# Performance work log

Hardware: AMD Instinct MI355X
Metric: run time of the kernel (lower is better)

The kernel has to match this reference:

```python
import jax, jax.numpy as jnp
import numpy as np

B, N, E = 4, 50000, 800000
C_IN, C_OUT, K = 64, 64, 3  # K = max_degree
AVG_DEG = 16.0


def setup_inputs() -> dict:
    key = jax.random.key(0)
    k1, k2, k3, k4, k5 = jax.random.split(key, 5)
    x = jax.random.normal(k1, (B, N, C_IN), dtype=jnp.float32)
    lap_rows = jax.random.randint(k2, (E,), 0, N)
    lap_cols = jax.random.randint(k3, (E,), 0, N)
    # scale so ||L|| stays O(1) and the Chebyshev recursion is stable
    lap_vals = jax.random.normal(k4, (E,), dtype=jnp.float32) / AVG_DEG
    weights = jax.random.normal(k5, (K + 1, C_IN, C_OUT), dtype=jnp.float32) * 0.1
    bias = jnp.full((C_OUT,), 0.1, dtype=jnp.float32)
    return dict(x=x, lap_rows=lap_rows, lap_cols=lap_cols,
                lap_vals=lap_vals, weights=weights, bias=bias)


def reference(x, lap_rows, lap_cols, lap_vals, weights, bias):
    # Sparse L @ X via edge list: gather source rows, scale, scatter-add to dest rows.
    def spmm_one(xb):  # xb: [N, C]
        return jax.ops.segment_sum(lap_vals[:, None] * xb[lap_cols], lap_rows,
                                   num_segments=N)

    spmm = jax.vmap(spmm_one)  # [B, N, C] -> [B, N, C]

    Tx0 = x
    out = jnp.einsum('bnc,co->bno', Tx0, weights[0])
    Tx1 = spmm(Tx0)
    out = out + jnp.einsum('bnc,co->bno', Tx1, weights[1])
    for k in range(2, K + 1):
        Tx2 = 2.0 * spmm(Tx1) - Tx0
        out = out + jnp.einsum('bnc,co->bno', Tx2, weights[k])
        Tx0, Tx1 = Tx1, Tx2
    return jax.nn.relu(out + bias)
```

## Files before the change

### kernel.cpp

```cpp
#include <hip/hip_runtime.h>


#define N_NODES 50000
#define N_EDGES 800000
#define BATCH 4
#define CH 64
#define BN (N_NODES * CH)
#define ROWS_TOTAL (BATCH * N_NODES)
#define NB 782
#define EPB 8192
#define SCT_BLOCKS ((N_EDGES + EPB - 1) / EPB)

typedef unsigned int uint;
typedef unsigned short ushort;
typedef unsigned char uchar;
typedef __attribute__((ext_vector_type(8))) short short8;
typedef __attribute__((ext_vector_type(4))) float f32x4;

__device__ __forceinline__ uint pack_bf16(float lo, float hi) {
  uint a = __float_as_uint(lo);
  uint b = __float_as_uint(hi);
  a = (a + 0x7fffu + ((a >> 16) & 1u)) >> 16;
  b = (b + 0x7fffu + ((b >> 16) & 1u)) >> 16;
  return a | (b << 16);
}
__device__ __forceinline__ ushort bf16one(float x) {
  uint a = __float_as_uint(x);
  a = (a + 0x7fffu + ((a >> 16) & 1u)) >> 16;
  return (ushort)a;
}
__device__ __forceinline__ uint q_u8(float v, float inv) {
  return (uint)((int)rintf(v * inv) + 128) & 0xffu;
}

__global__ __launch_bounds__(1024) void bucket_hist(const int* __restrict__ rows,
                                                    int* __restrict__ gcounts) {
  __shared__ int h[NB];
  for (int b = threadIdx.x; b < NB; b += 1024) h[b] = 0;
  __syncthreads();
  int base_e = blockIdx.x * EPB;
#pragma unroll
  for (int j = 0; j < EPB / 1024; ++j) {
    int e = base_e + j * 1024 + threadIdx.x;
    if (e < N_EDGES) atomicAdd(&h[rows[e] >> 6], 1);
  }
  __syncthreads();
  for (int b = threadIdx.x; b < NB; b += 1024)
    if (h[b]) atomicAdd(&gcounts[b], h[b]);
}

__global__ __launch_bounds__(1024) void bucket_scan(const int* __restrict__ gcounts,
                                                    int* __restrict__ bucket_base,
                                                    int* __restrict__ gcursor) {
  __shared__ int s[1024];
  int t = threadIdx.x;
  int v = (t < NB) ? gcounts[t] : 0;
  s[t] = v;
  __syncthreads();
  for (int off = 1; off < 1024; off <<= 1) {
    int tv = (t >= off) ? s[t - off] : 0;
    __syncthreads();
    s[t] += tv;
    __syncthreads();
  }
  int ex = s[t] - v;
  if (t < NB) { bucket_base[t] = ex; gcursor[t] = ex; }
  if (t == NB) bucket_base[NB] = N_EDGES;
}

__global__ __launch_bounds__(1024) void bucket_scatter(const int* __restrict__ rows,
                                                       const int* __restrict__ cols,
                                                       const float* __restrict__ vals,
                                                       int* __restrict__ gcursor,
                                                       uint2* __restrict__ staging) {
  __shared__ int lcur[NB];
  for (int b = threadIdx.x; b < NB; b += 1024) lcur[b] = 0;
  __syncthreads();
  int base_e = blockIdx.x * EPB;
#pragma unroll
  for (int j = 0; j < EPB / 1024; ++j) {
    int e = base_e + j * 1024 + threadIdx.x;
    if (e < N_EDGES) atomicAdd(&lcur[rows[e] >> 6], 1);
  }
  __syncthreads();
  for (int b = threadIdx.x; b < NB; b += 1024) {
    int c = lcur[b];
    lcur[b] = (c > 0) ? atomicAdd(&gcursor[b], c) : 0;
  }
  __syncthreads();
#pragma unroll
  for (int j = 0; j < EPB / 1024; ++j) {
    int e = base_e + j * 1024 + threadIdx.x;
    if (e < N_EDGES) {
      int r = rows[e];
      int pos = atomicAdd(&lcur[r >> 6], 1);
      staging[pos] = make_uint2((uint)cols[e] | ((uint)(r & 63) << 20),
                                __float_as_uint(vals[e]));
    }
  }
}

__global__ __launch_bounds__(256) void bucket_finalize(const int* __restrict__ bucket_base,
                                                       const uint2* __restrict__ staging,
                                                       uint2* __restrict__ pairs,
                                                       int* __restrict__ row_start) {
  int b = blockIdx.x;
  int seg0 = bucket_base[b], seg1 = bucket_base[b + 1];
  __shared__ int hist[64];
  __shared__ int cur[64];
  if (threadIdx.x < 64) hist[threadIdx.x] = 0;
  __syncthreads();
  for (int i = seg0 + threadIdx.x; i < seg1; i += 256)
    atomicAdd(&hist[staging[i].x >> 20], 1);
  __syncthreads();
  if (threadIdx.x < 64) {
    int v = hist[threadIdx.x];
    int sc = v;
#pragma unroll
    for (int off = 1; off < 64; off <<= 1) {
      int t = __shfl_up(sc, off, 64);
      if (threadIdx.x >= (unsigned)off) sc += t;
    }
    int start = seg0 + sc - v;
    cur[threadIdx.x] = start;
    int r = b * 64 + threadIdx.x;
    if (r < N_NODES) row_start[r] = start;
    if (r == N_NODES) row_start[N_NODES] = N_EDGES;
  }
  __syncthreads();
  for (int i = seg0 + threadIdx.x; i < seg1; i += 256) {
    uint2 eu = staging[i];
    int rl = eu.x >> 20;
    int pos = atomicAdd(&cur[rl], 1);
    pairs[pos] = make_uint2(eu.x & 0xFFFFFu, eu.y);
  }
}

__global__ __launch_bounds__(256) void wprep_kernel(const float* __restrict__ w,
                                                    ushort* __restrict__ wtT) {
  int t = blockIdx.x * 256 + threadIdx.x;
  if (t >= 64 * 256) return;
  int o = t >> 8, k = t & 255, m = k >> 6, c = k & 63;
  int idx = c * 64 + o;
  float v;
  if (m == 0)      v = w[idx] - w[2 * 4096 + idx];
  else if (m == 1) v = w[4096 + idx] - 3.0f * w[3 * 4096 + idx];
  else if (m == 2) v = 2.0f * w[2 * 4096 + idx];
  else             v = 4.0f * w[3 * 4096 + idx];
  wtT[t] = bf16one(v);
}

__global__ __launch_bounds__(256) void cvt_kernel(const float* __restrict__ in,
                                                  uint* __restrict__ xb,
                                                  uint* __restrict__ xu8w,
                                                  float* __restrict__ xsc) {
  int node = blockIdx.x * 4 + (threadIdx.x >> 6);
  int lane = threadIdx.x & 63;
  int b = lane >> 4;
  int ch4 = (lane & 15) * 4;
  float4 v = *reinterpret_cast<const float4*>(in + (size_t)b * BN + (size_t)node * 64 + ch4);
  uint2 bw = make_uint2(pack_bf16(v.x, v.y), pack_bf16(v.z, v.w));
  *reinterpret_cast<uint2*>(xb + (size_t)node * 128 + b * 32 + (lane & 15) * 2) = bw;
  float mx = fmaxf(fmaxf(fabsf(v.x), fabsf(v.y)), fmaxf(fabsf(v.z), fabsf(v.w)));
#pragma unroll
  for (int off = 1; off < 64; off <<= 1) mx = fmaxf(mx, __shfl_xor(mx, off, 64));
  float inv = mx > 0.f ? 127.0f / mx : 0.f;
  uint w8 = q_u8(v.x, inv) | (q_u8(v.y, inv) << 8) |
            (q_u8(v.z, inv) << 16) | (q_u8(v.w, inv) << 24);
  xu8w[(size_t)node * 64 + lane] = w8;
  if (lane == 0) xsc[node] = mx * (1.0f / 127.0f);
}

__device__ __forceinline__ void fma16_u8(float acc[16], float& sm, float m,
                                         const uint4& w) {
  const uint arr[4] = {w.x, w.y, w.z, w.w};
#pragma unroll
  for (int t = 0; t < 4; ++t) {
    uint u = arr[t];
    acc[t * 4 + 0] = fmaf(m, (float)(u & 0xffu),         acc[t * 4 + 0]);
    acc[t * 4 + 1] = fmaf(m, (float)((u >> 8) & 0xffu),  acc[t * 4 + 1]);
    acc[t * 4 + 2] = fmaf(m, (float)((u >> 16) & 0xffu), acc[t * 4 + 2]);
    acc[t * 4 + 3] = fmaf(m, (float)(u >> 24),           acc[t * 4 + 3]);
  }
  sm += m;
}

__device__ __forceinline__ void spmm_body(const int* __restrict__ row_start,
                                          const uint2* __restrict__ pairs,
                                          const uchar* __restrict__ src,
                                          const float* __restrict__ ssc,
                                          uchar* __restrict__ dst,
                                          float* __restrict__ dsc) {
  int row = blockIdx.x * 4 + (threadIdx.x >> 6);
  int lane = threadIdx.x & 63;
  int q = lane >> 4;
  int ql = lane & 15;
  const uchar* sb = src + ql * 16;
  int s = row_start[row], e = row_start[row + 1];
  float acc[16];
  float sm = 0.f;
#pragma unroll
  for (int j = 0; j < 16; ++j) acc[j] = 0.f;
  int i = s;
  for (; i + 7 < e; i += 8) {
    uint2 pa = pairs[i + q];
    uint2 pb = pairs[i + 4 + q];
    uint4 qa = *reinterpret_cast<const uint4*>(sb + (size_t)pa.x * 256);
    uint4 qb = *reinterpret_cast<const uint4*>(sb + (size_t)pb.x * 256);
    float ma = __uint_as_float(pa.y) * ssc[pa.x];
    float mb = __uint_as_float(pb.y) * ssc[pb.x];
    fma16_u8(acc, sm, ma, qa);
    fma16_u8(acc, sm, mb, qb);
  }
  for (; i < e; i += 4) {
    if (i + q < e) {
      uint2 p0 = pairs[i + q];
      uint4 q0 = *reinterpret_cast<const uint4*>(sb + (size_t)p0.x * 256);
      fma16_u8(acc, sm, __uint_as_float(p0.y) * ssc[p0.x], q0);
    }
  }
#pragma unroll
  for (int j = 0; j < 16; ++j) {
    acc[j] += __shfl_xor(acc[j], 16, 64);
    acc[j] += __shfl_xor(acc[j], 32, 64);
  }
  sm += __shfl_xor(sm, 16, 64);
  sm += __shfl_xor(sm, 32, 64);
#pragma unroll
  for (int j = 0; j < 16; ++j) acc[j] = fmaf(-128.f, sm, acc[j]);
  float mx = 0.f;
#pragma unroll
  for (int j = 0; j < 16; ++j) mx = fmaxf(mx, fabsf(acc[j]));
#pragma unroll
  for (int off = 1; off < 16; off <<= 1) mx = fmaxf(mx, __shfl_xor(mx, off, 64));
  if (lane < 16) {
    float inv = mx > 0.f ? 127.0f / mx : 0.f;
    uint w[4];
#pragma unroll
    for (int t = 0; t < 4; ++t) {
      w[t] = q_u8(acc[t * 4 + 0], inv) | (q_u8(acc[t * 4 + 1], inv) << 8) |
             (q_u8(acc[t * 4 + 2], inv) << 16) | (q_u8(acc[t * 4 + 3], inv) << 24);
    }
    *reinterpret_cast<uint4*>(dst + (size_t)row * 256 + ql * 16) =
        make_uint4(w[0], w[1], w[2], w[3]);
    if (lane == 0) dsc[row] = mx * (1.0f / 127.0f);
  }
}

__global__ __launch_bounds__(256) void spmm_s1(const int* __restrict__ rs,
                                               const uint2* __restrict__ pr,
                                               const uchar* __restrict__ src,
                                               const float* __restrict__ ssc,
                                               uchar* __restrict__ dst,
                                               float* __restrict__ dsc) {
  spmm_body(rs, pr, src, ssc, dst, dsc);
}
__global__ __launch_bounds__(256) void spmm_s2(const int* __restrict__ rs,
                                               const uint2* __restrict__ pr,
                                               const uchar* __restrict__ src,
                                               const float* __restrict__ ssc,
                                               uchar* __restrict__ dst,
                                               float* __restrict__ dsc) {
  spmm_body(rs, pr, src, ssc, dst, dsc);
}
__global__ __launch_bounds__(256) void spmm_s3(const int* __restrict__ rs,
                                               const uint2* __restrict__ pr,
                                               const uchar* __restrict__ src,
                                               const float* __restrict__ ssc,
                                               uchar* __restrict__ dst,
                                               float* __restrict__ dsc) {
  spmm_body(rs, pr, src, ssc, dst, dsc);
}

__device__ __forceinline__ short8 dequant8_u8(uint2 q, float sc, float nb) {
  float f0 = fmaf((float)(q.x & 0xffu),         sc, nb);
  float f1 = fmaf((float)((q.x >> 8) & 0xffu),  sc, nb);
  float f2 = fmaf((float)((q.x >> 16) & 0xffu), sc, nb);
  float f3 = fmaf((float)(q.x >> 24),           sc, nb);
  float f4 = fmaf((float)(q.y & 0xffu),         sc, nb);
  float f5 = fmaf((float)((q.y >> 8) & 0xffu),  sc, nb);
  float f6 = fmaf((float)((q.y >> 16) & 0xffu), sc, nb);
  float f7 = fmaf((float)(q.y >> 24),           sc, nb);
  uint4 v = make_uint4(pack_bf16(f0, f1), pack_bf16(f2, f3),
                       pack_bf16(f4, f5), pack_bf16(f6, f7));
  return __builtin_bit_cast(short8, v);
}

__global__ __launch_bounds__(256) void gemm4_mfma(
    const uint* __restrict__ A0bf,
    const uchar* __restrict__ A1u8, const float* __restrict__ A1sc,
    const uchar* __restrict__ A2u8, const float* __restrict__ A2sc,
    const uchar* __restrict__ A3u8, const float* __restrict__ A3sc,
    const uint* __restrict__ wtT,
    const float* __restrict__ bias, float* __restrict__ out) {
  __shared__ uint WS[64 * 132];
  __shared__ float bias_s[64];
  for (int w = threadIdx.x; w < 8192; w += 256)
    WS[(w >> 7) * 132 + (w & 127)] = wtT[w];
  if (threadIdx.x < 64) bias_s[threadIdx.x] = bias[threadIdx.x];
  __syncthreads();

  const int lane = threadIdx.x & 63;
  const int wv = threadIdx.x >> 6;
  const int r0 = blockIdx.x * 64 + wv * 16;
  const int c16 = lane & 15;
  const int hi = lane >> 4;

  const int ar = r0 + c16;
  const size_t arow_w = (size_t)ar * 32 + hi * 4;
  const size_t arow_b = (size_t)ar * 64 + hi * 8;
  const int nd = ar >> 2;
  const float sc1 = A1sc[nd];
  const float sc2 = A2sc[nd];
  const float sc3 = A3sc[nd];

  f32x4 acc[4] = {{0.f, 0.f, 0.f, 0.f}, {0.f, 0.f, 0.f, 0.f},
                  {0.f, 0.f, 0.f, 0.f}, {0.f, 0.f, 0.f, 0.f}};

#pragma unroll
  for (int ks = 0; ks < 8; ++ks) {
    short8 afrag;
    const int m = ks >> 1;
    if (m == 0) {
      uint4 av = *reinterpret_cast<const uint4*>(A0bf + arow_w + (ks & 1) * 16);
      afrag = __builtin_bit_cast(short8, av);
    } else if (m == 1) {
      uint2 qv = *reinterpret_cast<const uint2*>(A1u8 + arow_b + (ks & 1) * 32);
      afrag = dequant8_u8(qv, sc1, -128.f * sc1);
    } else if (m == 2) {
      uint2 qv = *reinterpret_cast<const uint2*>(A2u8 + arow_b + (ks & 1) * 32);
      afrag = dequant8_u8(qv, sc2, -128.f * sc2);
    } else {
      uint2 qv = *reinterpret_cast<const uint2*>(A3u8 + arow_b + (ks & 1) * 32);
      afrag = dequant8_u8(qv, sc3, -128.f * sc3);
    }
#pragma unroll
    for (int nt = 0; nt < 4; ++nt) {
      uint4 bv = *reinterpret_cast<const uint4*>(
          &WS[(nt * 16 + c16) * 132 + ks * 16 + hi * 4]);
      short8 bfrag = __builtin_bit_cast(short8, bv);
      acc[nt] = __builtin_amdgcn_mfma_f32_16x16x32_bf16(afrag, bfrag, acc[nt], 0, 0, 0);
    }
  }

#pragma unroll
  for (int nt = 0; nt < 4; ++nt) {
#pragma unroll
    for (int i = 0; i < 4; ++i) {
      int row = r0 + hi * 4 + i;
      int node = row >> 2, b = row & 3;
      int col = nt * 16 + c16;
      float v = acc[nt][i] + bias_s[col];
      out[(size_t)b * BN + (size_t)node * 64 + col] = fmaxf(v, 0.f);
    }
  }
}

extern "C" void kernel_launch(void* const* d_in, const int* in_sizes, int n_in,
                              void* d_out, int out_size, void* d_ws, size_t ws_size,
                              hipStream_t stream) {
  const float* x        = (const float*)d_in[0];
  const int*   lap_rows = (const int*)d_in[1];
  const int*   lap_cols = (const int*)d_in[2];
  const float* lap_vals = (const float*)d_in[3];
  const float* weights  = (const float*)d_in[4];
  const float* bias     = (const float*)d_in[5];
  float* out = (float*)d_out;

  char* ws = (char*)d_ws;
  size_t off = 0;
  auto alloc = [&](size_t bytes) {
    void* p = ws + off;
    off += (bytes + 255) & ~(size_t)255;
    return p;
  };
  int*    gcounts     = (int*)alloc((size_t)NB * 4);
  int*    gcursor     = (int*)alloc((size_t)NB * 4);
  int*    bucket_base = (int*)alloc((size_t)(NB + 1) * 4);
  int*    row_start   = (int*)alloc((size_t)(N_NODES + 1) * 4);
  uint2*  pairs       = (uint2*)alloc((size_t)N_EDGES * 8);
  uint2*  staging     = (uint2*)alloc((size_t)N_EDGES * 8);
  ushort* wtT         = (ushort*)alloc((size_t)64 * 256 * 2);
  uint*   xb          = (uint*)alloc((size_t)N_NODES * 128 * 4);
  uchar*  xu8         = (uchar*)alloc((size_t)N_NODES * 256);
  uchar*  S1u         = (uchar*)alloc((size_t)N_NODES * 256);
  uchar*  S2u         = (uchar*)alloc((size_t)N_NODES * 256);
  uchar*  S3u         = (uchar*)alloc((size_t)N_NODES * 256);
  float*  xsc         = (float*)alloc((size_t)N_NODES * 4);
  float*  S1sc        = (float*)alloc((size_t)N_NODES * 4);
  float*  S2sc        = (float*)alloc((size_t)N_NODES * 4);
  float*  S3sc        = (float*)alloc((size_t)N_NODES * 4);
  (void)ws_size; (void)in_sizes; (void)n_in; (void)out_size;

  wprep_kernel<<<64, 256, 0, stream>>>(weights, wtT);
  cvt_kernel<<<N_NODES / 4, 256, 0, stream>>>(x, xb, (uint*)xu8, xsc);
  hipMemsetAsync(gcounts, 0, (size_t)NB * 4, stream);
  bucket_hist<<<SCT_BLOCKS, 1024, 0, stream>>>(lap_rows, gcounts);
  bucket_scan<<<1, 1024, 0, stream>>>(gcounts, bucket_base, gcursor);
  bucket_scatter<<<SCT_BLOCKS, 1024, 0, stream>>>(lap_rows, lap_cols, lap_vals,
                                                  gcursor, staging);
  bucket_finalize<<<NB, 256, 0, stream>>>(bucket_base, staging, pairs, row_start);

  const int spmm_blocks = N_NODES / 4;

  spmm_s1<<<spmm_blocks, 256, 0, stream>>>(row_start, pairs, xu8, xsc, S1u, S1sc);
  spmm_s2<<<spmm_blocks, 256, 0, stream>>>(row_start, pairs, S1u, S1sc, S2u, S2sc);
  spmm_s3<<<spmm_blocks, 256, 0, stream>>>(row_start, pairs, S2u, S2sc, S3u, S3sc);
  gemm4_mfma<<<ROWS_TOTAL / 64, 256, 0, stream>>>(xb, S1u, S1sc, S2u, S2sc,
                                                  S3u, S3sc, (const uint*)wtT,
                                                  bias, out);
}
```

Measured before the change: 194.2 us.

## Split quantized feature rows into four channel slabs with per-slab scales

Node features are now quantized to u8 in four 64-byte slabs (per batch, 16 channels each), each with its own scale, stored as separate planes. The SpMM grid grows fourfold so each block handles one slab, gathering 4 bytes per lane instead of 16. A smaller working set per plane is meant to give better cache locality for the random gathers. The cost is more per-edge index and scale loads, and the GEMM has to read scales from several planes. Finer-grained scales also change the quantization precision.

```diff
diff --git a/kernel.cpp b/kernel.cpp
--- a/kernel.cpp
+++ b/kernel.cpp
@@ -10,6 +10,10 @@
 #define NB 782
 #define EPB 8192
 #define SCT_BLOCKS ((N_EDGES + EPB - 1) / EPB)
+#define NSUB 4
+#define SUB_BLOCKS (N_NODES / 4)
+#define RW (N_NODES * 16)
+#define RB (N_NODES * 64)
 
 typedef unsigned int uint;
 typedef unsigned short ushort;
@@ -157,117 +161,112 @@
   int node = blockIdx.x * 4 + (threadIdx.x >> 6);
   int lane = threadIdx.x & 63;
   int b = lane >> 4;
-  int ch4 = (lane & 15) * 4;
-  float4 v = *reinterpret_cast<const float4*>(in + (size_t)b * BN + (size_t)node * 64 + ch4);
+  int c4 = (lane & 15) * 4;
+  float4 v = *reinterpret_cast<const float4*>(in + (size_t)b * BN + (size_t)node * 64 + c4);
   uint2 bw = make_uint2(pack_bf16(v.x, v.y), pack_bf16(v.z, v.w));
   *reinterpret_cast<uint2*>(xb + (size_t)node * 128 + b * 32 + (lane & 15) * 2) = bw;
   float mx = fmaxf(fmaxf(fabsf(v.x), fabsf(v.y)), fmaxf(fabsf(v.z), fabsf(v.w)));
-#pragma unroll
-  for (int off = 1; off < 64; off <<= 1) mx = fmaxf(mx, __shfl_xor(mx, off, 64));
+  mx = fmaxf(mx, __shfl_xor(mx, 1, 64));
+  mx = fmaxf(mx, __shfl_xor(mx, 2, 64));
+  mx = fmaxf(mx, __shfl_xor(mx, 16, 64));
+  mx = fmaxf(mx, __shfl_xor(mx, 32, 64));
   float inv = mx > 0.f ? 127.0f / mx : 0.f;
   uint w8 = q_u8(v.x, inv) | (q_u8(v.y, inv) << 8) |
             (q_u8(v.z, inv) << 16) | (q_u8(v.w, inv) << 24);
-  xu8w[(size_t)node * 64 + lane] = w8;
-  if (lane == 0) xsc[node] = mx * (1.0f / 127.0f);
-}
-
-__device__ __forceinline__ void fma16_u8(float acc[16], float& sm, float m,
-                                         const uint4& w) {
-  const uint arr[4] = {w.x, w.y, w.z, w.w};
-#pragma unroll
-  for (int t = 0; t < 4; ++t) {
-    uint u = arr[t];
-    acc[t * 4 + 0] = fmaf(m, (float)(u & 0xffu),         acc[t * 4 + 0]);
-    acc[t * 4 + 1] = fmaf(m, (float)((u >> 8) & 0xffu),  acc[t * 4 + 1]);
-    acc[t * 4 + 2] = fmaf(m, (float)((u >> 16) & 0xffu), acc[t * 4 + 2]);
-    acc[t * 4 + 3] = fmaf(m, (float)(u >> 24),           acc[t * 4 + 3]);
-  }
+  int k = (lane & 15) >> 2;
+  xu8w[(size_t)k * RW + (size_t)node * 16 + b * 4 + (lane & 3)] = w8;
+  if ((lane & 51) == 0)
+    xsc[k * N_NODES + node] = mx * (1.0f / 127.0f);
+}
+
+__device__ __forceinline__ void fma4_u8(float acc[4], float& sm, float m, uint u) {
+  acc[0] = fmaf(m, (float)(u & 0xffu),         acc[0]);
+  acc[1] = fmaf(m, (float)((u >> 8) & 0xffu),  acc[1]);
+  acc[2] = fmaf(m, (float)((u >> 16) & 0xffu), acc[2]);
+  acc[3] = fmaf(m, (float)(u >> 24),           acc[3]);
   sm += m;
 }
 
 __device__ __forceinline__ void spmm_body(const int* __restrict__ row_start,
                                           const uint2* __restrict__ pairs,
-                                          const uchar* __restrict__ src,
+                                          const uint* __restrict__ src,
                                           const float* __restrict__ ssc,
-                                          uchar* __restrict__ dst,
+                                          uint* __restrict__ dst,
                                           float* __restrict__ dsc) {
-  int row = blockIdx.x * 4 + (threadIdx.x >> 6);
+  int k = blockIdx.x / SUB_BLOCKS;
+  int nc = blockIdx.x - k * SUB_BLOCKS;
+  int row = nc * 4 + (threadIdx.x >> 6);
   int lane = threadIdx.x & 63;
   int q = lane >> 4;
   int ql = lane & 15;
-  const uchar* sb = src + ql * 16;
+  const uint* srcl = src + (size_t)k * RW + ql;
+  const float* sscl = ssc + k * N_NODES;
   int s = row_start[row], e = row_start[row + 1];
-  float acc[16];
+  float acc[4] = {0.f, 0.f, 0.f, 0.f};
   float sm = 0.f;
-#pragma unroll
-  for (int j = 0; j < 16; ++j) acc[j] = 0.f;
   int i = s;
   for (; i + 7 < e; i += 8) {
     uint2 pa = pairs[i + q];
     uint2 pb = pairs[i + 4 + q];
-    uint4 qa = *reinterpret_cast<const uint4*>(sb + (size_t)pa.x * 256);
-    uint4 qb = *reinterpret_cast<const uint4*>(sb + (size_t)pb.x * 256);
-    float ma = __uint_as_float(pa.y) * ssc[pa.x];
-    float mb = __uint_as_float(pb.y) * ssc[pb.x];
-    fma16_u8(acc, sm, ma, qa);
-    fma16_u8(acc, sm, mb, qb);
+    uint ua = srcl[(size_t)pa.x * 16];
+    uint ub = srcl[(size_t)pb.x * 16];
+    float ma = __uint_as_float(pa.y) * sscl[pa.x];
+    float mb = __uint_as_float(pb.y) * sscl[pb.x];
+    fma4_u8(acc, sm, ma, ua);
+    fma4_u8(acc, sm, mb, ub);
   }
   for (; i < e; i += 4) {
     if (i + q < e) {
       uint2 p0 = pairs[i + q];
-      uint4 q0 = *reinterpret_cast<const uint4*>(sb + (size_t)p0.x * 256);
-      fma16_u8(acc, sm, __uint_as_float(p0.y) * ssc[p0.x], q0);
-    }
-  }
-#pragma unroll
-  for (int j = 0; j < 16; ++j) {
+      uint u0 = srcl[(size_t)p0.x * 16];
+      fma4_u8(acc, sm, __uint_as_float(p0.y) * sscl[p0.x], u0);
+    }
+  }
+#pragma unroll
+  for (int j = 0; j < 4; ++j) {
     acc[j] += __shfl_xor(acc[j], 16, 64);
     acc[j] += __shfl_xor(acc[j], 32, 64);
   }
   sm += __shfl_xor(sm, 16, 64);
   sm += __shfl_xor(sm, 32, 64);
 #pragma unroll
-  for (int j = 0; j < 16; ++j) acc[j] = fmaf(-128.f, sm, acc[j]);
-  float mx = 0.f;
-#pragma unroll
-  for (int j = 0; j < 16; ++j) mx = fmaxf(mx, fabsf(acc[j]));
-#pragma unroll
-  for (int off = 1; off < 16; off <<= 1) mx = fmaxf(mx, __shfl_xor(mx, off, 64));
+  for (int j = 0; j < 4; ++j) acc[j] = fmaf(-128.f, sm, acc[j]);
+  float mx = fmaxf(fmaxf(fabsf(acc[0]), fabsf(acc[1])),
+                   fmaxf(fabsf(acc[2]), fabsf(acc[3])));
+  mx = fmaxf(mx, __shfl_xor(mx, 1, 64));
+  mx = fmaxf(mx, __shfl_xor(mx, 2, 64));
+  mx = fmaxf(mx, __shfl_xor(mx, 4, 64));
+  mx = fmaxf(mx, __shfl_xor(mx, 8, 64));
   if (lane < 16) {
     float inv = mx > 0.f ? 127.0f / mx : 0.f;
-    uint w[4];
-#pragma unroll
-    for (int t = 0; t < 4; ++t) {
-      w[t] = q_u8(acc[t * 4 + 0], inv) | (q_u8(acc[t * 4 + 1], inv) << 8) |
-             (q_u8(acc[t * 4 + 2], inv) << 16) | (q_u8(acc[t * 4 + 3], inv) << 24);
-    }
-    *reinterpret_cast<uint4*>(dst + (size_t)row * 256 + ql * 16) =
-        make_uint4(w[0], w[1], w[2], w[3]);
-    if (lane == 0) dsc[row] = mx * (1.0f / 127.0f);
+    uint w = q_u8(acc[0], inv) | (q_u8(acc[1], inv) << 8) |
+             (q_u8(acc[2], inv) << 16) | (q_u8(acc[3], inv) << 24);
+    dst[(size_t)k * RW + (size_t)row * 16 + ql] = w;
+    if (lane == 0) dsc[k * N_NODES + row] = mx * (1.0f / 127.0f);
   }
 }
 
 __global__ __launch_bounds__(256) void spmm_s1(const int* __restrict__ rs,
                                                const uint2* __restrict__ pr,
-                                               const uchar* __restrict__ src,
+                                               const uint* __restrict__ src,
                                                const float* __restrict__ ssc,
-                                               uchar* __restrict__ dst,
+                                               uint* __restrict__ dst,
                                                float* __restrict__ dsc) {
   spmm_body(rs, pr, src, ssc, dst, dsc);
 }
 __global__ __launch_bounds__(256) void spmm_s2(const int* __restrict__ rs,
                                                const uint2* __restrict__ pr,
-                                               const uchar* __restrict__ src,
+                                               const uint* __restrict__ src,
                                                const float* __restrict__ ssc,
-                                               uchar* __restrict__ dst,
+                                               uint* __restrict__ dst,
                                                float* __restrict__ dsc) {
   spmm_body(rs, pr, src, ssc, dst, dsc);
 }
 __global__ __launch_bounds__(256) void spmm_s3(const int* __restrict__ rs,
                                                const uint2* __restrict__ pr,
-                                               const uchar* __restrict__ src,
+                                               const uint* __restrict__ src,
                                                const float* __restrict__ ssc,
-                                               uchar* __restrict__ dst,
+                                               uint* __restrict__ dst,
                                                float* __restrict__ dsc) {
   spmm_body(rs, pr, src, ssc, dst, dsc);
 }
@@ -305,14 +304,20 @@
   const int r0 = blockIdx.x * 64 + wv * 16;
   const int c16 = lane & 15;
   const int hi = lane >> 4;
+  const int hv = hi >> 1;
+  const int hb = (hi & 1) * 8;
 
   const int ar = r0 + c16;
   const size_t arow_w = (size_t)ar * 32 + hi * 4;
-  const size_t arow_b = (size_t)ar * 64 + hi * 8;
-  const int nd = ar >> 2;
-  const float sc1 = A1sc[nd];
-  const float sc2 = A2sc[nd];
-  const float sc3 = A3sc[nd];
+  const int node = ar >> 2, bb = ar & 3;
+  const size_t abase = (size_t)node * 64 + bb * 16 + hb;
+
+  float s1r0 = A1sc[node], s1r1 = A1sc[N_NODES + node],
+        s1r2 = A1sc[2 * N_NODES + node], s1r3 = A1sc[3 * N_NODES + node];
+  float s2r0 = A2sc[node], s2r1 = A2sc[N_NODES + node],
+        s2r2 = A2sc[2 * N_NODES + node], s2r3 = A2sc[3 * N_NODES + node];
+  float s3r0 = A3sc[node], s3r1 = A3sc[N_NODES + node],
+        s3r2 = A3sc[2 * N_NODES + node], s3r3 = A3sc[3 * N_NODES + node];
 
   f32x4 acc[4] = {{0.f, 0.f, 0.f, 0.f}, {0.f, 0.f, 0.f, 0.f},
                   {0.f, 0.f, 0.f, 0.f}, {0.f, 0.f, 0.f, 0.f}};
@@ -321,18 +326,19 @@
   for (int ks = 0; ks < 8; ++ks) {
     short8 afrag;
     const int m = ks >> 1;
+    const int kk = ks & 1;
     if (m == 0) {
-      uint4 av = *reinterpret_cast<const uint4*>(A0bf + arow_w + (ks & 1) * 16);
+      uint4 av = *reinterpret_cast<const uint4*>(A0bf + arow_w + kk * 16);
       afrag = __builtin_bit_cast(short8, av);
-    } else if (m == 1) {
-      uint2 qv = *reinterpret_cast<const uint2*>(A1u8 + arow_b + (ks & 1) * 32);
-      afrag = dequant8_u8(qv, sc1, -128.f * sc1);
-    } else if (m == 2) {
-      uint2 qv = *reinterpret_cast<const uint2*>(A2u8 + arow_b + (ks & 1) * 32);
-      afrag = dequant8_u8(qv, sc2, -128.f * sc2);
     } else {
-      uint2 qv = *reinterpret_cast<const uint2*>(A3u8 + arow_b + (ks & 1) * 32);
-      afrag = dequant8_u8(qv, sc3, -128.f * sc3);
+      const uchar* Au = (m == 1) ? A1u8 : (m == 2) ? A2u8 : A3u8;
+      float sc;
+      if (m == 1) sc = kk ? (hv ? s1r3 : s1r2) : (hv ? s1r1 : s1r0);
+      else if (m == 2) sc = kk ? (hv ? s2r3 : s2r2) : (hv ? s2r1 : s2r0);
+      else sc = kk ? (hv ? s3r3 : s3r2) : (hv ? s3r1 : s3r0);
+      const int kreg = kk * 2 + hv;
+      uint2 qv = *reinterpret_cast<const uint2*>(Au + (size_t)kreg * RB + abase);
+      afrag = dequant8_u8(qv, sc, -128.f * sc);
     }
 #pragma unroll
     for (int nt = 0; nt < 4; ++nt) {
@@ -348,10 +354,10 @@
 #pragma unroll
     for (int i = 0; i < 4; ++i) {
       int row = r0 + hi * 4 + i;
-      int node = row >> 2, b = row & 3;
+      int nd2 = row >> 2, b2 = row & 3;
       int col = nt * 16 + c16;
       float v = acc[nt][i] + bias_s[col];
-      out[(size_t)b * BN + (size_t)node * 64 + col] = fmaxf(v, 0.f);
+      out[(size_t)b2 * BN + (size_t)nd2 * 64 + col] = fmaxf(v, 0.f);
     }
   }
 }
@@ -382,18 +388,18 @@
   uint2*  staging     = (uint2*)alloc((size_t)N_EDGES * 8);
   ushort* wtT         = (ushort*)alloc((size_t)64 * 256 * 2);
   uint*   xb          = (uint*)alloc((size_t)N_NODES * 128 * 4);
-  uchar*  xu8         = (uchar*)alloc((size_t)N_NODES * 256);
-  uchar*  S1u         = (uchar*)alloc((size_t)N_NODES * 256);
-  uchar*  S2u         = (uchar*)alloc((size_t)N_NODES * 256);
-  uchar*  S3u         = (uchar*)alloc((size_t)N_NODES * 256);
-  float*  xsc         = (float*)alloc((size_t)N_NODES * 4);
-  float*  S1sc        = (float*)alloc((size_t)N_NODES * 4);
-  float*  S2sc        = (float*)alloc((size_t)N_NODES * 4);
-  float*  S3sc        = (float*)alloc((size_t)N_NODES * 4);
+  uint*   xu8         = (uint*)alloc((size_t)NSUB * RW * 4);
+  uint*   S1u         = (uint*)alloc((size_t)NSUB * RW * 4);
+  uint*   S2u         = (uint*)alloc((size_t)NSUB * RW * 4);
+  uint*   S3u         = (uint*)alloc((size_t)NSUB * RW * 4);
+  float*  xsc         = (float*)alloc((size_t)NSUB * N_NODES * 4);
+  float*  S1sc        = (float*)alloc((size_t)NSUB * N_NODES * 4);
+  float*  S2sc        = (float*)alloc((size_t)NSUB * N_NODES * 4);
+  float*  S3sc        = (float*)alloc((size_t)NSUB * N_NODES * 4);
   (void)ws_size; (void)in_sizes; (void)n_in; (void)out_size;
 
   wprep_kernel<<<64, 256, 0, stream>>>(weights, wtT);
-  cvt_kernel<<<N_NODES / 4, 256, 0, stream>>>(x, xb, (uint*)xu8, xsc);
+  cvt_kernel<<<N_NODES / 4, 256, 0, stream>>>(x, xb, xu8, xsc);
   hipMemsetAsync(gcounts, 0, (size_t)NB * 4, stream);
   bucket_hist<<<SCT_BLOCKS, 1024, 0, stream>>>(lap_rows, gcounts);
   bucket_scan<<<1, 1024, 0, stream>>>(gcounts, bucket_base, gcursor);
@@ -401,12 +407,13 @@
                                                   gcursor, staging);
   bucket_finalize<<<NB, 256, 0, stream>>>(bucket_base, staging, pairs, row_start);
 
-  const int spmm_blocks = N_NODES / 4;
-
-  spmm_s1<<<spmm_blocks, 256, 0, stream>>>(row_start, pairs, xu8, xsc, S1u, S1sc);
-  spmm_s2<<<spmm_blocks, 256, 0, stream>>>(row_start, pairs, S1u, S1sc, S2u, S2sc);
-  spmm_s3<<<spmm_blocks, 256, 0, stream>>>(row_start, pairs, S2u, S2sc, S3u, S3sc);
-  gemm4_mfma<<<ROWS_TOTAL / 64, 256, 0, stream>>>(xb, S1u, S1sc, S2u, S2sc,
-                                                  S3u, S3sc, (const uint*)wtT,
-                                                  bias, out);
-}
+  const int spmm_grid = NSUB * SUB_BLOCKS;
+
+  spmm_s1<<<spmm_grid, 256, 0, stream>>>(row_start, pairs, xu8, xsc, S1u, S1sc);
+  spmm_s2<<<spmm_grid, 256, 0, stream>>>(row_start, pairs, S1u, S1sc, S2u, S2sc);
+  spmm_s3<<<spmm_grid, 256, 0, stream>>>(row_start, pairs, S2u, S2sc, S3u, S3sc);
+  gemm4_mfma<<<ROWS_TOTAL / 64, 256, 0, stream>>>(xb, (const uchar*)S1u, S1sc,
+                                                  (const uchar*)S2u, S2sc,
+                                                  (const uchar*)S3u, S3sc,
+                                                  (const uint*)wtT, bias, out);
+}
```

After: 336.3 us. 1.73x slower.

## Prescale edge values by source scales and drop bf16 copy of input

Applied to the files above, without the earlier changes.

Adds a scale_pairs kernel that multiplies each edge value by its source node's quantization scale before each SpMM. The SpMM inner loop then no longer performs a random gather of the scale array. The input is also stored only as u8, in a batch-major layout, and the GEMM dequantizes term 0 the same way as the other terms, so the bf16 x buffer is no longer written or read. The cost is three extra passes over the 6.4MB edge array, and term 0 now feeds the MMA from 8-bit values instead of bf16, which lowers its precision.

```diff
diff --git a/kernel.cpp b/kernel.cpp
--- a/kernel.cpp
+++ b/kernel.cpp
@@ -134,6 +134,15 @@
     int pos = atomicAdd(&cur[rl], 1);
     pairs[pos] = make_uint2(eu.x & 0xFFFFFu, eu.y);
   }
+}
+
+__global__ __launch_bounds__(256) void scale_pairs(const uint2* __restrict__ raw,
+                                                   const float* __restrict__ sc,
+                                                   uint2* __restrict__ outp) {
+  int e = blockIdx.x * 256 + threadIdx.x;
+  if (e >= N_EDGES) return;
+  uint2 p = raw[e];
+  outp[e] = make_uint2(p.x, __float_as_uint(__uint_as_float(p.y) * sc[p.x]));
 }
 
 __global__ __launch_bounds__(256) void wprep_kernel(const float* __restrict__ w,
@@ -151,23 +160,20 @@
 }
 
 __global__ __launch_bounds__(256) void cvt_kernel(const float* __restrict__ in,
-                                                  uint* __restrict__ xb,
                                                   uint* __restrict__ xu8w,
                                                   float* __restrict__ xsc) {
   int node = blockIdx.x * 4 + (threadIdx.x >> 6);
   int lane = threadIdx.x & 63;
   int b = lane >> 4;
-  int ch4 = (lane & 15) * 4;
-  float4 v = *reinterpret_cast<const float4*>(in + (size_t)b * BN + (size_t)node * 64 + ch4);
-  uint2 bw = make_uint2(pack_bf16(v.x, v.y), pack_bf16(v.z, v.w));
-  *reinterpret_cast<uint2*>(xb + (size_t)node * 128 + b * 32 + (lane & 15) * 2) = bw;
+  int c4 = (lane & 15) * 4;
+  float4 v = *reinterpret_cast<const float4*>(in + (size_t)b * BN + (size_t)node * 64 + c4);
   float mx = fmaxf(fmaxf(fabsf(v.x), fabsf(v.y)), fmaxf(fabsf(v.z), fabsf(v.w)));
 #pragma unroll
   for (int off = 1; off < 64; off <<= 1) mx = fmaxf(mx, __shfl_xor(mx, off, 64));
   float inv = mx > 0.f ? 127.0f / mx : 0.f;
   uint w8 = q_u8(v.x, inv) | (q_u8(v.y, inv) << 8) |
             (q_u8(v.z, inv) << 16) | (q_u8(v.w, inv) << 24);
-  xu8w[(size_t)node * 64 + lane] = w8;
+  xu8w[(size_t)node * 64 + b * 16 + (lane & 15)] = w8;
   if (lane == 0) xsc[node] = mx * (1.0f / 127.0f);
 }
 
@@ -188,7 +194,6 @@
 __device__ __forceinline__ void spmm_body(const int* __restrict__ row_start,
                                           const uint2* __restrict__ pairs,
                                           const uchar* __restrict__ src,
-                                          const float* __restrict__ ssc,
                                           uchar* __restrict__ dst,
                                           float* __restrict__ dsc) {
   int row = blockIdx.x * 4 + (threadIdx.x >> 6);
@@ -207,16 +212,14 @@
     uint2 pb = pairs[i + 4 + q];
     uint4 qa = *reinterpret_cast<const uint4*>(sb + (size_t)pa.x * 256);
     uint4 qb = *reinterpret_cast<const uint4*>(sb + (size_t)pb.x * 256);
-    float ma = __uint_as_float(pa.y) * ssc[pa.x];
-    float mb = __uint_as_float(pb.y) * ssc[pb.x];
-    fma16_u8(acc, sm, ma, qa);
-    fma16_u8(acc, sm, mb, qb);
+    fma16_u8(acc, sm, __uint_as_float(pa.y), qa);
+    fma16_u8(acc, sm, __uint_as_float(pb.y), qb);
   }
   for (; i < e; i += 4) {
     if (i + q < e) {
       uint2 p0 = pairs[i + q];
       uint4 q0 = *reinterpret_cast<const uint4*>(sb + (size_t)p0.x * 256);
-      fma16_u8(acc, sm, __uint_as_float(p0.y) * ssc[p0.x], q0);
+      fma16_u8(acc, sm, __uint_as_float(p0.y), q0);
     }
   }
 #pragma unroll
@@ -250,26 +253,23 @@
 __global__ __launch_bounds__(256) void spmm_s1(const int* __restrict__ rs,
                                                const uint2* __restrict__ pr,
                                                const uchar* __restrict__ src,
-                                               const float* __restrict__ ssc,
                                                uchar* __restrict__ dst,
                                                float* __restrict__ dsc) {
-  spmm_body(rs, pr, src, ssc, dst, dsc);
+  spmm_body(rs, pr, src, dst, dsc);
 }
 __global__ __launch_bounds__(256) void spmm_s2(const int* __restrict__ rs,
                                                const uint2* __restrict__ pr,
                                                const uchar* __restrict__ src,
-                                               const float* __restrict__ ssc,
                                                uchar* __restrict__ dst,
                                                float* __restrict__ dsc) {
-  spmm_body(rs, pr, src, ssc, dst, dsc);
+  spmm_body(rs, pr, src, dst, dsc);
 }
 __global__ __launch_bounds__(256) void spmm_s3(const int* __restrict__ rs,
                                                const uint2* __restrict__ pr,
                                                const uchar* __restrict__ src,
-                                               const float* __restrict__ ssc,
                                                uchar* __restrict__ dst,
                                                float* __restrict__ dsc) {
-  spmm_body(rs, pr, src, ssc, dst, dsc);
+  spmm_body(rs, pr, src, dst, dsc);
 }
 
 __device__ __forceinline__ short8 dequant8_u8(uint2 q, float sc, float nb) {
@@ -287,7 +287,7 @@
 }
 
 __global__ __launch_bounds__(256) void gemm4_mfma(
-    const uint* __restrict__ A0bf,
+    const uchar* __restrict__ A0u8, const float* __restrict__ A0sc,
     const uchar* __restrict__ A1u8, const float* __restrict__ A1sc,
     const uchar* __restrict__ A2u8, const float* __restrict__ A2sc,
     const uchar* __restrict__ A3u8, const float* __restrict__ A3sc,
@@ -307,9 +307,9 @@
   const int hi = lane >> 4;
 
   const int ar = r0 + c16;
-  const size_t arow_w = (size_t)ar * 32 + hi * 4;
   const size_t arow_b = (size_t)ar * 64 + hi * 8;
   const int nd = ar >> 2;
+  const float sc0 = A0sc[nd];
   const float sc1 = A1sc[nd];
   const float sc2 = A2sc[nd];
   const float sc3 = A3sc[nd];
@@ -319,21 +319,11 @@
 
 #pragma unroll
   for (int ks = 0; ks < 8; ++ks) {
-    short8 afrag;
     const int m = ks >> 1;
-    if (m == 0) {
-      uint4 av = *reinterpret_cast<const uint4*>(A0bf + arow_w + (ks & 1) * 16);
-      afrag = __builtin_bit_cast(short8, av);
-    } else if (m == 1) {
-      uint2 qv = *reinterpret_cast<const uint2*>(A1u8 + arow_b + (ks & 1) * 32);
-      afrag = dequant8_u8(qv, sc1, -128.f * sc1);
-    } else if (m == 2) {
-      uint2 qv = *reinterpret_cast<const uint2*>(A2u8 + arow_b + (ks & 1) * 32);
-      afrag = dequant8_u8(qv, sc2, -128.f * sc2);
-    } else {
-      uint2 qv = *reinterpret_cast<const uint2*>(A3u8 + arow_b + (ks & 1) * 32);
-      afrag = dequant8_u8(qv, sc3, -128.f * sc3);
-    }
+    const uchar* Au = (m == 0) ? A0u8 : (m == 1) ? A1u8 : (m == 2) ? A2u8 : A3u8;
+    const float sc = (m == 0) ? sc0 : (m == 1) ? sc1 : (m == 2) ? sc2 : sc3;
+    uint2 qv = *reinterpret_cast<const uint2*>(Au + arow_b + (ks & 1) * 32);
+    short8 afrag = dequant8_u8(qv, sc, -128.f * sc);
 #pragma unroll
     for (int nt = 0; nt < 4; ++nt) {
       uint4 bv = *reinterpret_cast<const uint4*>(
@@ -378,10 +368,11 @@
   int*    gcursor     = (int*)alloc((size_t)NB * 4);
   int*    bucket_base = (int*)alloc((size_t)(NB + 1) * 4);
   int*    row_start   = (int*)alloc((size_t)(N_NODES + 1) * 4);
-  uint2*  pairs       = (uint2*)alloc((size_t)N_EDGES * 8);
+  uint2*  pairs_raw   = (uint2*)alloc((size_t)N_EDGES * 8);
+  uint2*  pairs_a     = (uint2*)alloc((size_t)N_EDGES * 8);
+  uint2*  pairs_b     = (uint2*)alloc((size_t)N_EDGES * 8);
   uint2*  staging     = (uint2*)alloc((size_t)N_EDGES * 8);
   ushort* wtT         = (ushort*)alloc((size_t)64 * 256 * 2);
-  uint*   xb          = (uint*)alloc((size_t)N_NODES * 128 * 4);
   uchar*  xu8         = (uchar*)alloc((size_t)N_NODES * 256);
   uchar*  S1u         = (uchar*)alloc((size_t)N_NODES * 256);
   uchar*  S2u         = (uchar*)alloc((size_t)N_NODES * 256);
@@ -393,20 +384,24 @@
   (void)ws_size; (void)in_sizes; (void)n_in; (void)out_size;
 
   wprep_kernel<<<64, 256, 0, stream>>>(weights, wtT);
-  cvt_kernel<<<N_NODES / 4, 256, 0, stream>>>(x, xb, (uint*)xu8, xsc);
+  cvt_kernel<<<N_NODES / 4, 256, 0, stream>>>(x, (uint*)xu8, xsc);
   hipMemsetAsync(gcounts, 0, (size_t)NB * 4, stream);
   bucket_hist<<<SCT_BLOCKS, 1024, 0, stream>>>(lap_rows, gcounts);
   bucket_scan<<<1, 1024, 0, stream>>>(gcounts, bucket_base, gcursor);
   bucket_scatter<<<SCT_BLOCKS, 1024, 0, stream>>>(lap_rows, lap_cols, lap_vals,
                                                   gcursor, staging);
-  bucket_finalize<<<NB, 256, 0, stream>>>(bucket_base, staging, pairs, row_start);
+  bucket_finalize<<<NB, 256, 0, stream>>>(bucket_base, staging, pairs_raw, row_start);
 
   const int spmm_blocks = N_NODES / 4;
-
-  spmm_s1<<<spmm_blocks, 256, 0, stream>>>(row_start, pairs, xu8, xsc, S1u, S1sc);
-  spmm_s2<<<spmm_blocks, 256, 0, stream>>>(row_start, pairs, S1u, S1sc, S2u, S2sc);
-  spmm_s3<<<spmm_blocks, 256, 0, stream>>>(row_start, pairs, S2u, S2sc, S3u, S3sc);
-  gemm4_mfma<<<ROWS_TOTAL / 64, 256, 0, stream>>>(xb, S1u, S1sc, S2u, S2sc,
+  const int sp_blocks = (N_EDGES + 255) / 256;
+
+  scale_pairs<<<sp_blocks, 256, 0, stream>>>(pairs_raw, xsc, pairs_a);
+  spmm_s1<<<spmm_blocks, 256, 0, stream>>>(row_start, pairs_a, xu8, S1u, S1sc);
+  scale_pairs<<<sp_blocks, 256, 0, stream>>>(pairs_raw, S1sc, pairs_b);
+  spmm_s2<<<spmm_blocks, 256, 0, stream>>>(row_start, pairs_b, S1u, S2u, S2sc);
+  scale_pairs<<<sp_blocks, 256, 0, stream>>>(pairs_raw, S2sc, pairs_a);
+  spmm_s3<<<spmm_blocks, 256, 0, stream>>>(row_start, pairs_a, S2u, S3u, S3sc);
+  gemm4_mfma<<<ROWS_TOTAL / 64, 256, 0, stream>>>(xu8, xsc, S1u, S1sc, S2u, S2sc,
                                                   S3u, S3sc, (const uint*)wtT,
                                                   bias, out);
 }
```

Measured after the change: 205.5 us. 1.06x slower.
